# Kernel optimization log

Hardware: AMD Instinct MI355X
Metric: run time of the kernel (lower is better)

The kernel has to match this reference:

```python
import jax, jax.numpy as jnp
import numpy as np

CHUNK_SIZE = 2048
LOCAL_WINDOW = 384
CHUNK_LEN = CHUNK_SIZE - LOCAL_WINDOW  # 1664
N_HEADS = 16
N_KV_HEADS = 4
HEAD_DIM = 128
HIDDEN = 2048
SEQ = 3 * CHUNK_LEN  # 4992
NEG_INF = -1e9


def _cos_sin(positions, dim=HEAD_DIM, base=10000.0):
    inv = 1.0 / (base ** (np.arange(0, dim, 2, dtype=np.float64) / dim))
    freqs = np.outer(np.asarray(positions, np.float64), inv)
    emb = np.concatenate([freqs, freqs], axis=-1)
    return jnp.asarray(np.cos(emb), jnp.float32), jnp.asarray(np.sin(emb), jnp.float32)


def setup_inputs() -> dict:
    key = jax.random.key(0)
    ks = jax.random.split(key, 5)
    hidden_states = jax.random.normal(ks[0], (1, SEQ, HIDDEN), jnp.float32) * 0.02
    position_ids = jnp.arange(SEQ, dtype=jnp.int32)[None, :]
    q_cos, q_sin = _cos_sin(np.arange(SEQ))                 # intra rotary (positions mod chunk_len)
    qc_cos, qc_sin = _cos_sin(np.arange(SEQ) + CHUNK_LEN)   # cross-chunk rotary variant
    k_cos, k_sin = _cos_sin(np.arange(SEQ))                 # key rotary (absolute positions)
    kv_dim = N_KV_HEADS * HEAD_DIM
    Wq = jax.random.normal(ks[1], (N_HEADS * HEAD_DIM, HIDDEN), jnp.float32) * 0.02
    Wk = jax.random.normal(ks[2], (kv_dim, HIDDEN), jnp.float32) * 0.02
    Wv = jax.random.normal(ks[3], (kv_dim, HIDDEN), jnp.float32) * 0.02
    Wo = jax.random.normal(ks[4], (HIDDEN, N_HEADS * HEAD_DIM), jnp.float32) * 0.02
    return dict(hidden_states=hidden_states, position_ids=position_ids,
                q_cos=q_cos, q_sin=q_sin, qc_cos=qc_cos, qc_sin=qc_sin,
                k_cos=k_cos, k_sin=k_sin, Wq=Wq, Wk=Wk, Wv=Wv, Wo=Wo)


def _rotate_half(x):
    x1, x2 = jnp.split(x, 2, axis=-1)
    return jnp.concatenate([-x2, x1], axis=-1)


def _rope(x, cos_t, sin_t, pid):
    # x: [b,h,s,d], pid: [b,s] -> cos/sin [b,1,s,d]
    cos = cos_t[pid][:, None]
    sin = sin_t[pid][:, None]
    return x * cos + _rotate_half(x) * sin


def _attn(q, k, v, causal):
    # flash-attn semantics: scale = head_dim**-0.5, returns output and fp32 LSE [b,h,q]
    scale = q.shape[-1] ** -0.5
    s = jnp.einsum('bhqd,bhkd->bhqk', q, k).astype(jnp.float32) * scale
    if causal:
        L, K = s.shape[-2], s.shape[-1]
        mask = jnp.tril(jnp.ones((L, K), bool))
        s = jnp.where(mask, s, NEG_INF)
    lse = jax.nn.logsumexp(s, axis=-1)
    p = jax.nn.softmax(s, axis=-1).astype(q.dtype)
    out = jnp.einsum('bhqk,bhkd->bhqd', p, v)
    return out, lse


def _merge(parts):
    # LSE-weighted merge of partial attention outputs (weights detached, as in torch)
    outs = jnp.stack([p[0] for p in parts])       # [n,b,h,q,d]
    lses = jnp.stack([p[1] for p in parts])       # [n,b,h,q] fp32
    w = jax.lax.stop_gradient(jax.nn.softmax(lses, axis=0))
    return jnp.sum(outs * w[..., None].astype(outs.dtype), axis=0)


def _forward(hidden_states, position_ids, q_cos, q_sin, qc_cos, qc_sin, k_cos, k_sin, Wq, Wk, Wv, Wo):
    b, s, _ = hidden_states.shape
    q = (hidden_states @ Wq.T).reshape(b, s, N_HEADS, HEAD_DIM).transpose(0, 2, 1, 3)
    k = (hidden_states @ Wk.T).reshape(b, s, N_KV_HEADS, HEAD_DIM).transpose(0, 2, 1, 3)
    v = (hidden_states @ Wv.T).reshape(b, s, N_KV_HEADS, HEAD_DIM).transpose(0, 2, 1, 3)

    k = _rope(k, k_cos, k_sin, position_ids)
    pid = position_ids % CHUNK_LEN

    groups = N_HEADS // N_KV_HEADS
    k = jnp.repeat(k, groups, axis=1)
    v = jnp.repeat(v, groups, axis=1)

    n_chunks = s // CHUNK_LEN
    # chunk 0: intra causal only
    q0 = _rope(q[:, :, :CHUNK_LEN], q_cos, q_sin, pid[:, :CHUNK_LEN])
    out0, _ = _attn(q0, k[:, :, :CHUNK_LEN], v[:, :, :CHUNK_LEN], causal=True)
    outs = [out0]
    for i in range(1, n_chunks):
        b0 = i * CHUNK_LEN
        e = b0 + CHUNK_LEN
        qi = q[:, :, b0:e]
        pid_c = pid[:, b0:e]
        parts = [_attn(_rope(qi, q_cos, q_sin, pid_c), k[:, :, b0:e], v[:, :, b0:e], causal=True),
                 _attn(_rope(qi, qc_cos, qc_sin, pid_c), k[:, :, b0 - CHUNK_LEN:b0], v[:, :, b0 - CHUNK_LEN:b0], causal=False)]
        if b0 - CHUNK_LEN > 0:
            pid_i = jnp.full_like(pid_c, CHUNK_LEN - 1)
            parts.append(_attn(_rope(qi, qc_cos, qc_sin, pid_i), k[:, :, :b0 - CHUNK_LEN], v[:, :, :b0 - CHUNK_LEN], causal=False))
        outs.append(_merge(parts))
    attn_out = jnp.concatenate(outs, axis=2)                      # [b,h,s,d]
    attn_out = attn_out.transpose(0, 2, 1, 3).reshape(b, s, -1)   # [b,s,h*d]
    return attn_out @ Wo.T


def reference(hidden_states, position_ids, q_cos, q_sin, qc_cos, qc_sin, k_cos, k_sin, Wq, Wk, Wv, Wo):
    return _forward(hidden_states, position_ids, q_cos, q_sin, qc_cos, qc_sin, k_cos, k_sin, Wq, Wk, Wv, Wo)
```

## Files before the change

kernel.cpp:

```cpp
#include <hip/hip_runtime.h>

typedef unsigned short u16;
typedef unsigned int u32;
typedef __attribute__((ext_vector_type(8))) __bf16 bf16x8;
typedef __attribute__((ext_vector_type(4))) float f32x4;
typedef __attribute__((ext_vector_type(16))) float f32x16;

#define CLEN 1664
#define SEQL 4992
#define NHEADS 16
#define HD 128
#define HID 2048
#define KVD 512
#define SCALE 0.08838834764831845f
#define NPARTS 672

__device__ __forceinline__ u16 f2bf(float f) {
  union { float f; u32 u; } v; v.f = f;
  u32 u = v.u;
  return (u16)((u + 0x7FFFu + ((u >> 16) & 1u)) >> 16);
}
__device__ __forceinline__ float bf2f(u16 h) {
  union { u32 u; float f; } v; v.u = (u32)h << 16;
  return v.f;
}
__device__ __forceinline__ f32x4 mfma16(bf16x8 a, bf16x8 b, f32x4 c) {
  return __builtin_amdgcn_mfma_f32_16x16x32_bf16(a, b, c, 0, 0, 0);
}
__device__ __forceinline__ f32x16 mfma32(bf16x8 a, bf16x8 b, f32x16 c) {
  return __builtin_amdgcn_mfma_f32_32x32x16_bf16(a, b, c, 0, 0, 0);
}
__device__ __forceinline__ u32 cvtpk(float lo, float hi) {
  u32 r;
  asm("v_cvt_pk_bf16_f32 %0, %1, %2" : "=v"(r) : "v"(lo), "v"(hi));
  return r;
}
__device__ __forceinline__ void gload_lds16(const u16* g, u16* l) {
  __builtin_amdgcn_global_load_lds((const __attribute__((address_space(1))) void*)g,
                                   (__attribute__((address_space(3))) void*)l, 16, 0, 0);
}

#define CVT_Q0 2555904
#define CVT_Q1 1048576
#define CVT_Q2 262144
#define CVT_Q3 262144
#define CVT_Q4 1048576
__device__ __forceinline__ void cvt4(const float* s, u16* d, int q) {
  float4 v = *(const float4*)(s + (size_t)q * 4);
  uint2 p;
  p.x = (u32)f2bf(v.x) | ((u32)f2bf(v.y) << 16);
  p.y = (u32)f2bf(v.z) | ((u32)f2bf(v.w) << 16);
  *(uint2*)(d + (size_t)q * 4) = p;
}
__global__ void cvt_all_kernel(const float* __restrict__ hidden, const float* __restrict__ Wq,
                               const float* __restrict__ Wk, const float* __restrict__ Wv,
                               const float* __restrict__ Wo, u16* __restrict__ h_bf,
                               u16* __restrict__ Wqkv, u16* __restrict__ Wo_bf,
                               u32* __restrict__ cnt) {
  int q = blockIdx.x * blockDim.x + threadIdx.x;
  if (q == 0) *cnt = 0;
  if (q < CVT_Q0) { cvt4(hidden, h_bf, q); return; }
  q -= CVT_Q0;
  if (q < CVT_Q1) { cvt4(Wq, Wqkv, q); return; }
  q -= CVT_Q1;
  if (q < CVT_Q2) { cvt4(Wk, Wqkv + 2048 * 2048, q); return; }
  q -= CVT_Q2;
  if (q < CVT_Q3) { cvt4(Wv, Wqkv + 2560 * 2048, q); return; }
  q -= CVT_Q3;
  if (q < CVT_Q4) cvt4(Wo, Wo_bf, q);
}

#define RP_N0 1277952
#define RP_N1 851968
#define RP_N2 425984
#define RP_N3 319488
__device__ __forceinline__ void rope8(const u16* __restrict__ src, u16* __restrict__ dst,
                                      const float* __restrict__ ctab, const float* __restrict__ stab,
                                      int s, int dstrow, int col, int rowlen, int pid, float scl) {
  const int dh = col & 127;
  const bool hih = dh >= 64;
  const u16* rowp = src + (size_t)s * rowlen;
  union { uint4 u; u16 h[8]; } X, P, O;
  X.u = *(const uint4*)(rowp + col);
  P.u = *(const uint4*)(rowp + col + (hih ? -64 : 64));
  const float* cp = ctab + pid * 128 + dh;
  const float* sp = stab + pid * 128 + dh;
#pragma unroll
  for (int j = 0; j < 8; ++j) {
    float v = bf2f(X.h[j]) * cp[j] + (hih ? bf2f(P.h[j]) : -bf2f(P.h[j])) * sp[j];
    O.h[j] = f2bf(v * scl);
  }
  *(uint4*)(dst + (size_t)dstrow * rowlen + col) = O.u;
}
__global__ void rope_all_kernel(const u16* __restrict__ q_tmp, const u16* __restrict__ k_tmp,
                                u16* __restrict__ qa, u16* __restrict__ qb, u16* __restrict__ qf,
                                u16* __restrict__ k_bf, const float* __restrict__ q_cos,
                                const float* __restrict__ q_sin, const float* __restrict__ qc_cos,
                                const float* __restrict__ qc_sin, const float* __restrict__ k_cos,
                                const float* __restrict__ k_sin) {
  int o = blockIdx.x * blockDim.x + threadIdx.x;
  if (o < RP_N0) {
    int r = o >> 8, col = (o & 255) * 8;
    rope8(q_tmp, qa, q_cos, q_sin, r, r, col, 2048, r % CLEN, SCALE);
    return;
  }
  o -= RP_N0;
  if (o < RP_N1) {
    int r = o >> 8, col = (o & 255) * 8, s = CLEN + r;
    rope8(q_tmp, qb, qc_cos, qc_sin, s, r, col, 2048, s % CLEN, SCALE);
    return;
  }
  o -= RP_N1;
  if (o < RP_N2) {
    int r = o >> 8, col = (o & 255) * 8, s = 2 * CLEN + r;
    rope8(q_tmp, qf, qc_cos, qc_sin, s, r, col, 2048, CLEN - 1, SCALE);
    return;
  }
  o -= RP_N2;
  if (o < RP_N3) {
    int r = o >> 6, col = (o & 63) * 8;
    rope8(k_tmp, k_bf, k_cos, k_sin, r, r, col, 512, r, 1.0f);
  }
}

__global__ __launch_bounds__(256) void gemm_qkv(const u16* __restrict__ A, const u16* __restrict__ B,
                                                u16* __restrict__ q_tmp, u16* __restrict__ k_tmp,
                                                u16* __restrict__ vT) {
  __shared__ __align__(16) u16 Al[128 * 64];
  __shared__ __align__(16) u16 Bl[128 * 64];
  const int K = HID;
  const int t = threadIdx.x;
  const int lane = t & 63, wid = t >> 6;
  const int g = lane >> 4, c = lane & 15;
  const int wr = wid >> 1, wc = wid & 1;
  const int m0 = blockIdx.x * 128, n0 = blockIdx.y * 128;

  f32x4 acc[4][4];
#pragma unroll
  for (int m = 0; m < 4; ++m)
#pragma unroll
    for (int n = 0; n < 4; ++n) acc[m][n] = (f32x4){0.f, 0.f, 0.f, 0.f};

  const int srow = t >> 3;
  const int scol = (t & 7) * 8;
  for (int k0 = 0; k0 < K; k0 += 64) {
    __syncthreads();
#pragma unroll
    for (int i = 0; i < 4; ++i) {
      const int r = i * 32 + srow;
      gload_lds16(A + (size_t)(m0 + r) * K + k0 + scol, Al + i * 2048 + wid * 512);
      gload_lds16(B + (size_t)(n0 + r) * K + k0 + scol, Bl + i * 2048 + wid * 512);
    }
    __syncthreads();
#pragma unroll
    for (int kk = 0; kk < 2; ++kk) {
      bf16x8 af[4], bfr[4];
#pragma unroll
      for (int m = 0; m < 4; ++m)
        af[m] = *(const bf16x8*)(Al + (wr * 64 + m * 16 + c) * 64 + kk * 32 + g * 8);
#pragma unroll
      for (int n = 0; n < 4; ++n)
        bfr[n] = *(const bf16x8*)(Bl + (wc * 64 + n * 16 + c) * 64 + kk * 32 + g * 8);
#pragma unroll
      for (int m = 0; m < 4; ++m)
#pragma unroll
        for (int n = 0; n < 4; ++n)
          acc[m][n] = mfma16(af[m], bfr[n], acc[m][n]);
    }
  }
#pragma unroll
  for (int m = 0; m < 4; ++m)
#pragma unroll
    for (int n = 0; n < 4; ++n)
#pragma unroll
      for (int j = 0; j < 4; ++j) {
        const int row = m0 + wr * 64 + m * 16 + 4 * g + j;
        const int col = n0 + wc * 64 + n * 16 + c;
        const float v = acc[m][n][j];
        if (n0 < 2048)       q_tmp[(size_t)row * 2048 + col] = f2bf(v);
        else if (n0 < 2560)  k_tmp[(size_t)row * 512 + (col - 2048)] = f2bf(v);
        else                 vT[(size_t)(col - 2560) * SEQL + row] = f2bf(v);
      }
}

__global__ __launch_bounds__(256) void gemm_o(const u16* __restrict__ A, const u16* __restrict__ B,
                                              float* __restrict__ Cf) {
  __shared__ __align__(16) u16 Al[128 * 64];
  __shared__ __align__(16) u16 Bl[128 * 64];
  const int K = HID, N = HID;
  const int t = threadIdx.x;
  const int lane = t & 63, wid = t >> 6;
  const int g = lane >> 4, c = lane & 15;
  const int wr = wid >> 1, wc = wid & 1;
  const int m0 = blockIdx.x * 128, n0 = blockIdx.y * 128;

  f32x4 acc[4][4];
#pragma unroll
  for (int m = 0; m < 4; ++m)
#pragma unroll
    for (int n = 0; n < 4; ++n) acc[m][n] = (f32x4){0.f, 0.f, 0.f, 0.f};

  const int srow = t >> 3;
  const int scol = (t & 7) * 8;
  for (int k0 = 0; k0 < K; k0 += 64) {
    __syncthreads();
#pragma unroll
    for (int i = 0; i < 4; ++i) {
      const int r = i * 32 + srow;
      gload_lds16(A + (size_t)(m0 + r) * K + k0 + scol, Al + i * 2048 + wid * 512);
      gload_lds16(B + (size_t)(n0 + r) * K + k0 + scol, Bl + i * 2048 + wid * 512);
    }
    __syncthreads();
#pragma unroll
    for (int kk = 0; kk < 2; ++kk) {
      bf16x8 af[4], bfr[4];
#pragma unroll
      for (int m = 0; m < 4; ++m)
        af[m] = *(const bf16x8*)(Al + (wr * 64 + m * 16 + c) * 64 + kk * 32 + g * 8);
#pragma unroll
      for (int n = 0; n < 4; ++n)
        bfr[n] = *(const bf16x8*)(Bl + (wc * 64 + n * 16 + c) * 64 + kk * 32 + g * 8);
#pragma unroll
      for (int m = 0; m < 4; ++m)
#pragma unroll
        for (int n = 0; n < 4; ++n)
          acc[m][n] = mfma16(af[m], bfr[n], acc[m][n]);
    }
  }
#pragma unroll
  for (int m = 0; m < 4; ++m)
#pragma unroll
    for (int n = 0; n < 4; ++n)
#pragma unroll
      for (int j = 0; j < 4; ++j) {
        const int row = m0 + wr * 64 + m * 16 + 4 * g + j;
        const int col = n0 + wc * 64 + n * 16 + c;
        Cf[(size_t)row * N + col] = acc[m][n][j];
      }
}

__global__ __launch_bounds__(512, 4) void attn_kernel(
    const u16* __restrict__ qa, const u16* __restrict__ qbuf, const u16* __restrict__ qf,
    const u16* __restrict__ kbf, const u16* __restrict__ vT,
    u16* __restrict__ Opart, float* __restrict__ lseout, u32* __restrict__ cnt) {
  __shared__ __align__(16) u16 Klds[2][64 * 128];
  __shared__ __align__(16) u16 Vlds[2][128 * 64];
  __shared__ float albuf[8][32];
  __shared__ int wsh;

  const int t = threadIdx.x, wid = t >> 6, lane = t & 63;
  const int ql = lane & 31, hi = lane >> 5;
  const int ksr = t >> 4, ksc = t & 15;
  const int vsr = t >> 3, vsc = t & 7;

  for (;;) {
    __syncthreads();
    if (t == 0) wsh = (int)atomicAdd(cnt, 1u);
    __syncthreads();
    const int w = wsh;
    if (w >= NPARTS) break;

    const int head = w & 15, rk = w >> 4;
    int chunk, seg, qb;
    if (rk < 21) {
      const int part = rk / 7; qb = rk % 7;
      chunk = (part == 0) ? 1 : 2;
      seg = (part == 2) ? 1 : 0;
    } else if (rk < 24) {
      chunk = rk - 21; seg = chunk; qb = 6;
    } else {
      const int g2 = rk - 24;
      qb = 5 - g2 / 3; chunk = g2 % 3; seg = chunk;
    }
    const bool causal = (seg == chunk);
    const int nt = causal ? ((qb == 6) ? 26 : (4 * qb + 4)) : 26;
    const int slot = causal ? 0 : ((chunk - seg == 1) ? 1 : 2);
    const int kvh = head >> 2;
    const int kvbase = seg * CLEN;
    const int qcb = qb * 256 + wid * 32;
    const int qpos = qcb + ql;
    const bool wact = qcb < CLEN;

    const u16* qp; int qoff;
    if (causal)                { qp = qa;   qoff = 0; }
    else if (chunk - seg == 1) { qp = qbuf; qoff = CLEN; }
    else                       { qp = qf;   qoff = 2 * CLEN; }

    bf16x8 aq[8];
    {
      const int qrow = wact ? (chunk * CLEN + qpos - qoff) : 0;
      const u16* qptr = qp + (size_t)qrow * HID + head * HD + hi * 8;
#pragma unroll
      for (int ck = 0; ck < 8; ++ck) aq[ck] = *(const bf16x8*)(qptr + ck * 16);
    }

    float l_r = 0.f;
    f32x16 oacc[4];
#pragma unroll
    for (int db = 0; db < 4; ++db)
#pragma unroll
      for (int r = 0; r < 16; ++r) oacc[db][r] = 0.f;

    auto stage = [&](int b, int kt) {
      const int kv0 = kt * 64;
#pragma unroll
      for (int i = 0; i < 2; ++i) {
        const int rr = ksr + 32 * i;
        const int gs = ksc ^ (rr & 7);
        gload_lds16(kbf + (size_t)(kvbase + kv0 + rr) * KVD + kvh * HD + gs * 8,
                    &Klds[b][i * 4096 + wid * 512]);
      }
#pragma unroll
      for (int i = 0; i < 2; ++i) {
        const int rr = vsr + 64 * i;
        const int gs = vsc ^ (rr & 7);
        gload_lds16(vT + (size_t)(kvh * HD + rr) * SEQL + kvbase + kv0 + gs * 8,
                    &Vlds[b][i * 4096 + wid * 512]);
      }
    };

    stage(0, 0);
    int cur = 0;
    for (int kt = 0; kt < nt; ++kt) {
      if (kt + 1 < nt) {
        stage(cur ^ 1, kt + 1);
        asm volatile("s_waitcnt vmcnt(4)" ::: "memory");
      } else {
        asm volatile("s_waitcnt vmcnt(0)" ::: "memory");
      }
      __builtin_amdgcn_s_barrier();
      const int kv0 = kt * 64;
      const u16* Kb = &Klds[cur][0];
      const u16* Vb = &Vlds[cur][0];
#pragma unroll
      for (int s = 0; s < 2; ++s) {
        if (wact && !(causal && kv0 + 32 * s > qcb + 31)) {
          f32x16 sacc;
#pragma unroll
          for (int r = 0; r < 16; ++r) sacc[r] = 0.f;
          const int kr = 32 * s + ql;
          const int r7 = lane & 7;
#pragma unroll
          for (int ck = 0; ck < 8; ++ck) {
            bf16x8 kb = *(const bf16x8*)(Kb + kr * 128 + (((2 * ck + hi) ^ r7) * 8));
            sacc = mfma32(kb, aq[ck], sacc);
          }
          float e[16];
          float rs = 0.f;
#pragma unroll
          for (int r = 0; r < 16; ++r) {
            const int kvp = kv0 + 32 * s + (r & 3) + 8 * (r >> 2) + 4 * hi;
            float ev = sacc[r];
            if (causal && kvp > qpos) ev = -1e30f;
            e[r] = __expf(ev);
            rs += e[r];
          }
          rs += __shfl_xor(rs, 32);
          l_r += rs;
          u32 wp[8];
#pragma unroll
          for (int j = 0; j < 8; ++j) wp[j] = cvtpk(e[2 * j], e[2 * j + 1]);
#pragma unroll
          for (int ks = 0; ks < 2; ++ks) {
            union { uint4 u; bf16x8 v; } pa;
            pa.u.x = wp[4 * ks]; pa.u.y = wp[4 * ks + 1];
            pa.u.z = wp[4 * ks + 2]; pa.u.w = wp[4 * ks + 3];
            const int g4a = 8 * s + 4 * ks + hi;
            const int sw = (lane & 7) << 1;
#pragma unroll
            for (int db = 0; db < 4; ++db) {
              const int vrow = 32 * db + ql;
              const uint2 v0 = *(const uint2*)(Vb + vrow * 64 + ((g4a ^ sw) * 4));
              const uint2 v1 = *(const uint2*)(Vb + vrow * 64 + (((g4a + 2) ^ sw) * 4));
              union { uint4 u; bf16x8 v; } bv;
              bv.u.x = v0.x; bv.u.y = v0.y; bv.u.z = v1.x; bv.u.w = v1.y;
              oacc[db] = mfma32(pa.v, bv.v, oacc[db]);
            }
          }
        }
      }
      __builtin_amdgcn_s_barrier();
      cur ^= 1;
    }
    if (wact) {
      const float linv = 1.0f / l_r;
      albuf[wid][ql] = linv;
      asm volatile("s_waitcnt lgkmcnt(0)" ::: "memory");
#pragma unroll
      for (int r = 0; r < 16; ++r) {
        const int rrow = (r & 3) + 8 * (r >> 2) + 4 * hi;
        const float li = albuf[wid][rrow];
        const size_t grow = (size_t)(chunk * CLEN + qcb + rrow);
#pragma unroll
        for (int db = 0; db < 4; ++db)
          Opart[((size_t)slot * SEQL + grow) * HID + head * HD + db * 32 + ql] =
              f2bf(oacc[db][r] * li);
      }
      if (hi == 0)
        lseout[((size_t)slot * NHEADS + head) * SEQL + chunk * CLEN + qcb + ql] = __logf(l_r);
    }
  }
}

__global__ void merge_kernel(const u16* __restrict__ Opart, const float* __restrict__ lse,
                             u16* __restrict__ amrg) {
  const int idx = blockIdx.x * blockDim.x + threadIdx.x;
  const int row = idx >> 8;
  const int col = (idx & 255) * 8;
  const int head = col >> 7;
  const int np = row / CLEN + 1;
  float ls[3];
  float mx = -1e30f;
  for (int i = 0; i < np; ++i) {
    ls[i] = lse[((size_t)i * NHEADS + head) * SEQL + row];
    mx = fmaxf(mx, ls[i]);
  }
  float wsum = 0.f;
  for (int i = 0; i < np; ++i) { ls[i] = __expf(ls[i] - mx); wsum += ls[i]; }
  const float inv = 1.0f / wsum;
  float acc[8];
#pragma unroll
  for (int j = 0; j < 8; ++j) acc[j] = 0.f;
  for (int i = 0; i < np; ++i) {
    union { uint4 u; u16 h[8]; } X;
    X.u = *(const uint4*)(Opart + ((size_t)i * SEQL + row) * (size_t)HID + col);
#pragma unroll
    for (int j = 0; j < 8; ++j) acc[j] += ls[i] * bf2f(X.h[j]);
  }
  union { uint4 u; u16 h[8]; } O;
#pragma unroll
  for (int j = 0; j < 8; ++j) O.h[j] = f2bf(acc[j] * inv);
  *(uint4*)(amrg + (size_t)row * 2048 + col) = O.u;
}

extern "C" void kernel_launch(void* const* d_in, const int* in_sizes, int n_in,
                              void* d_out, int out_size, void* d_ws, size_t ws_size,
                              hipStream_t stream) {
  (void)in_sizes; (void)n_in; (void)out_size; (void)ws_size;
  const float* hidden = (const float*)d_in[0];
  const float* q_cos = (const float*)d_in[2];
  const float* q_sin = (const float*)d_in[3];
  const float* qc_cos = (const float*)d_in[4];
  const float* qc_sin = (const float*)d_in[5];
  const float* k_cos = (const float*)d_in[6];
  const float* k_sin = (const float*)d_in[7];
  const float* Wq = (const float*)d_in[8];
  const float* Wk = (const float*)d_in[9];
  const float* Wv = (const float*)d_in[10];
  const float* Wo = (const float*)d_in[11];
  float* out = (float*)d_out;

  char* ws = (char*)d_ws;
  u16* Wo_bf = (u16*)(ws + 0);
  u16* qa    = (u16*)(ws + 8388608);
  u16* qb    = (u16*)(ws + 28835840);
  u16* qf    = (u16*)(ws + 42467328);
  u16* k_bf  = (u16*)(ws + 49283072);
  u16* vT    = (u16*)(ws + 54394880);
  char* BIG  = ws + 59506688;
  u16* h_bf  = (u16*)(BIG + 0);
  u16* Wqkv  = (u16*)(BIG + 20447232);
  u16* q_tmp = (u16*)(BIG + 33030144);
  u16* k_tmp = (u16*)(BIG + 53477376);
  u16* Opart = (u16*)(BIG + 0);
  float* lse = (float*)(BIG + 61341696);
  u32* cnt   = (u32*)(BIG + 61341696 + 958464);
  u16* amrg  = qa;

  cvt_all_kernel<<<dim3(20224), dim3(256), 0, stream>>>(hidden, Wq, Wk, Wv, Wo, h_bf, Wqkv, Wo_bf, cnt);
  gemm_qkv<<<dim3(SEQL / 128, 24), 256, 0, stream>>>(h_bf, Wqkv, q_tmp, k_tmp, vT);
  rope_all_kernel<<<dim3(11232), dim3(256), 0, stream>>>(q_tmp, k_tmp, qa, qb, qf, k_bf,
                                                         q_cos, q_sin, qc_cos, qc_sin, k_cos, k_sin);
  attn_kernel<<<dim3(512), dim3(512), 0, stream>>>(qa, qb, qf, k_bf, vT, Opart, lse, cnt);
  merge_kernel<<<dim3(SEQL), dim3(256), 0, stream>>>(Opart, lse, amrg);
  gemm_o<<<dim3(SEQL / 128, HID / 128), 256, 0, stream>>>(amrg, Wo_bf, out);
}
```

Measured before the change: 554.5 us.

## Make GEMM and attention work assignment XCD-aware and coalesce attention output stores

```diff
diff --git a/kernel.cpp b/kernel.cpp
--- a/kernel.cpp
+++ b/kernel.cpp
@@ -13,7 +13,7 @@
 #define HID 2048
 #define KVD 512
 #define SCALE 0.08838834764831845f
-#define NPARTS 672
+#define QPARTS 84
 
 __device__ __forceinline__ u16 f2bf(float f) {
   union { float f; u32 u; } v; v.f = f;
@@ -58,7 +58,7 @@
                                u16* __restrict__ Wqkv, u16* __restrict__ Wo_bf,
                                u32* __restrict__ cnt) {
   int q = blockIdx.x * blockDim.x + threadIdx.x;
-  if (q == 0) *cnt = 0;
+  if (q < 8) cnt[q * 64] = 0;
   if (q < CVT_Q0) { cvt4(hidden, h_bf, q); return; }
   q -= CVT_Q0;
   if (q < CVT_Q1) { cvt4(Wq, Wqkv, q); return; }
@@ -133,7 +133,9 @@
   const int lane = t & 63, wid = t >> 6;
   const int g = lane >> 4, c = lane & 15;
   const int wr = wid >> 1, wc = wid & 1;
-  const int m0 = blockIdx.x * 128, n0 = blockIdx.y * 128;
+  const int bid = blockIdx.x;
+  const int wg = (bid & 7) * 117 + (bid >> 3);
+  const int m0 = (wg % 39) * 128, n0 = (wg / 39) * 128;
 
   f32x4 acc[4][4];
 #pragma unroll
@@ -141,13 +143,12 @@
 #pragma unroll
     for (int n = 0; n < 4; ++n) acc[m][n] = (f32x4){0.f, 0.f, 0.f, 0.f};
 
-  const int srow = t >> 3;
   const int scol = (t & 7) * 8;
   for (int k0 = 0; k0 < K; k0 += 64) {
     __syncthreads();
 #pragma unroll
     for (int i = 0; i < 4; ++i) {
-      const int r = i * 32 + srow;
+      const int r = i * 32 + (t >> 3);
       gload_lds16(A + (size_t)(m0 + r) * K + k0 + scol, Al + i * 2048 + wid * 512);
       gload_lds16(B + (size_t)(n0 + r) * K + k0 + scol, Bl + i * 2048 + wid * 512);
     }
@@ -192,7 +193,9 @@
   const int lane = t & 63, wid = t >> 6;
   const int g = lane >> 4, c = lane & 15;
   const int wr = wid >> 1, wc = wid & 1;
-  const int m0 = blockIdx.x * 128, n0 = blockIdx.y * 128;
+  const int bid = blockIdx.x;
+  const int wg = (bid & 7) * 78 + (bid >> 3);
+  const int m0 = (wg % 39) * 128, n0 = (wg / 39) * 128;
 
   f32x4 acc[4][4];
 #pragma unroll
@@ -200,13 +203,12 @@
 #pragma unroll
     for (int n = 0; n < 4; ++n) acc[m][n] = (f32x4){0.f, 0.f, 0.f, 0.f};
 
-  const int srow = t >> 3;
   const int scol = (t & 7) * 8;
   for (int k0 = 0; k0 < K; k0 += 64) {
     __syncthreads();
 #pragma unroll
     for (int i = 0; i < 4; ++i) {
-      const int r = i * 32 + srow;
+      const int r = i * 32 + (t >> 3);
       gload_lds16(A + (size_t)(m0 + r) * K + k0 + scol, Al + i * 2048 + wid * 512);
       gload_lds16(B + (size_t)(n0 + r) * K + k0 + scol, Bl + i * 2048 + wid * 512);
     }
@@ -243,24 +245,25 @@
     const u16* __restrict__ qa, const u16* __restrict__ qbuf, const u16* __restrict__ qf,
     const u16* __restrict__ kbf, const u16* __restrict__ vT,
     u16* __restrict__ Opart, float* __restrict__ lseout, u32* __restrict__ cnt) {
-  __shared__ __align__(16) u16 Klds[2][64 * 128];
-  __shared__ __align__(16) u16 Vlds[2][128 * 64];
-  __shared__ float albuf[8][32];
+  __shared__ __align__(16) u16 smem[2 * 16384];
   __shared__ int wsh;
 
   const int t = threadIdx.x, wid = t >> 6, lane = t & 63;
   const int ql = lane & 31, hi = lane >> 5;
+  const int qid = blockIdx.x & 7;
+  const int kvh = qid >> 1, headpar = qid & 1;
   const int ksr = t >> 4, ksc = t & 15;
   const int vsr = t >> 3, vsc = t & 7;
 
   for (;;) {
     __syncthreads();
-    if (t == 0) wsh = (int)atomicAdd(cnt, 1u);
+    if (t == 0) wsh = (int)atomicAdd(cnt + qid * 64, 1u);
     __syncthreads();
     const int w = wsh;
-    if (w >= NPARTS) break;
-
-    const int head = w & 15, rk = w >> 4;
+    if (w >= QPARTS) break;
+
+    const int head = kvh * 4 + ((w & 1) << 1) + headpar;
+    const int rk = w >> 1;
     int chunk, seg, qb;
     if (rk < 21) {
       const int part = rk / 7; qb = rk % 7;
@@ -275,7 +278,6 @@
     const bool causal = (seg == chunk);
     const int nt = causal ? ((qb == 6) ? 26 : (4 * qb + 4)) : 26;
     const int slot = causal ? 0 : ((chunk - seg == 1) ? 1 : 2);
-    const int kvh = head >> 2;
     const int kvbase = seg * CLEN;
     const int qcb = qb * 256 + wid * 32;
     const int qpos = qcb + ql;
@@ -308,14 +310,14 @@
         const int rr = ksr + 32 * i;
         const int gs = ksc ^ (rr & 7);
         gload_lds16(kbf + (size_t)(kvbase + kv0 + rr) * KVD + kvh * HD + gs * 8,
-                    &Klds[b][i * 4096 + wid * 512]);
+                    smem + b * 16384 + i * 4096 + wid * 512);
       }
 #pragma unroll
       for (int i = 0; i < 2; ++i) {
         const int rr = vsr + 64 * i;
         const int gs = vsc ^ (rr & 7);
         gload_lds16(vT + (size_t)(kvh * HD + rr) * SEQL + kvbase + kv0 + gs * 8,
-                    &Vlds[b][i * 4096 + wid * 512]);
+                    smem + b * 16384 + 8192 + i * 4096 + wid * 512);
       }
     };
 
@@ -330,8 +332,8 @@
       }
       __builtin_amdgcn_s_barrier();
       const int kv0 = kt * 64;
-      const u16* Kb = &Klds[cur][0];
-      const u16* Vb = &Vlds[cur][0];
+      const u16* Kb = smem + cur * 16384;
+      const u16* Vb = smem + cur * 16384 + 8192;
 #pragma unroll
       for (int s = 0; s < 2; ++s) {
         if (wact && !(causal && kv0 + 32 * s > qcb + 31)) {
@@ -384,17 +386,23 @@
     }
     if (wact) {
       const float linv = 1.0f / l_r;
-      albuf[wid][ql] = linv;
-      asm volatile("s_waitcnt lgkmcnt(0)" ::: "memory");
+      u16* scr = smem + wid * 4096;
 #pragma unroll
       for (int r = 0; r < 16; ++r) {
         const int rrow = (r & 3) + 8 * (r >> 2) + 4 * hi;
-        const float li = albuf[wid][rrow];
-        const size_t grow = (size_t)(chunk * CLEN + qcb + rrow);
+        const float li = __shfl(linv, rrow);
 #pragma unroll
         for (int db = 0; db < 4; ++db)
-          Opart[((size_t)slot * SEQL + grow) * HID + head * HD + db * 32 + ql] =
-              f2bf(oacc[db][r] * li);
+          scr[rrow * 128 + db * 32 + ql] = f2bf(oacc[db][r] * li);
+      }
+      asm volatile("s_waitcnt lgkmcnt(0)" ::: "memory");
+      const int rcol = lane & 15;
+#pragma unroll
+      for (int p = 0; p < 8; ++p) {
+        const int row = p * 4 + (lane >> 4);
+        uint4 v = *(const uint4*)(scr + row * 128 + rcol * 8);
+        const size_t grow = (size_t)(chunk * CLEN + qcb + row);
+        *(uint4*)(Opart + ((size_t)slot * SEQL + grow) * HID + head * HD + rcol * 8) = v;
       }
       if (hi == 0)
         lseout[((size_t)slot * NHEADS + head) * SEQL + chunk * CLEN + qcb + ql] = __logf(l_r);
@@ -468,10 +476,10 @@
   u16* amrg  = qa;
 
   cvt_all_kernel<<<dim3(20224), dim3(256), 0, stream>>>(hidden, Wq, Wk, Wv, Wo, h_bf, Wqkv, Wo_bf, cnt);
-  gemm_qkv<<<dim3(SEQL / 128, 24), 256, 0, stream>>>(h_bf, Wqkv, q_tmp, k_tmp, vT);
+  gemm_qkv<<<dim3(936), 256, 0, stream>>>(h_bf, Wqkv, q_tmp, k_tmp, vT);
   rope_all_kernel<<<dim3(11232), dim3(256), 0, stream>>>(q_tmp, k_tmp, qa, qb, qf, k_bf,
                                                          q_cos, q_sin, qc_cos, qc_sin, k_cos, k_sin);
   attn_kernel<<<dim3(512), dim3(512), 0, stream>>>(qa, qb, qf, k_bf, vT, Opart, lse, cnt);
   merge_kernel<<<dim3(SEQL), dim3(256), 0, stream>>>(Opart, lse, amrg);
-  gemm_o<<<dim3(SEQL / 128, HID / 128), 256, 0, stream>>>(amrg, Wo_bf, out);
-}
+  gemm_o<<<dim3(624), 256, 0, stream>>>(amrg, Wo_bf, out);
+}
```

Result: slower. 573.1 us (+3.4%).
